# Kernel tuning notes

Measured on AMD Instinct MI355X. Metric: run time of the kernel, lower is better.

The kernel has to match this reference:

```python
import jax, jax.numpy as jnp
import numpy as np

N = 50000      # nodes
E = 800000     # edges (avg degree 16)
IN = 128       # in_channels
C = 64         # hidden_channels (per-head out channels)
H = 8          # heads


def _lin(key, fan_in, fan_out):
    kw, kb = jax.random.split(key)
    scale = 1.0 / np.sqrt(fan_in)
    W = jax.random.uniform(kw, (fan_in, fan_out), jnp.float32, -scale, scale)
    b = jax.random.uniform(kb, (fan_out,), jnp.float32, -scale, scale)
    return W, b


def setup_inputs() -> dict:
    key = jax.random.key(0)
    ks = jax.random.split(key, 16)
    inp = {
        'x': jax.random.normal(ks[0], (N, IN), jnp.float32),
        'edge_index': jax.random.randint(ks[1], (2, E), 0, N, jnp.int64),
    }
    # layer 0: IN -> H*C (concat), layer 1: H*C -> H*C (concat), layer 2: H*C -> C (heads=1)
    dims = [(IN, H * C, H * C), (H * C, H * C, H * C), (H * C, C, C)]
    k = 2
    for i, (fi, fqkv, fskip) in enumerate(dims):
        for nm, fo in (('Wq', fqkv), ('Wk', fqkv), ('Wv', fqkv), ('Ws', fskip)):
            W, b = _lin(ks[k], fi, fo)
            inp[f'{nm}{i}'] = W
            inp[f'b{nm[1]}{i}'] = b
            k += 1
    return inp


def _conv(x, src, dst, Wq, bq, Wk, bk, Wv, bv, Ws, bs, heads, ch, concat):
    n = x.shape[0]
    q = (x @ Wq + bq).reshape(n, heads, ch)   # [N,H,C]
    k = (x @ Wk + bk).reshape(n, heads, ch)
    v = (x @ Wv + bv).reshape(n, heads, ch)
    # per-edge attention logits: [E,H]
    alpha = jnp.einsum('ehc,ehc->eh', q[dst], k[src]) / (ch ** 0.5)
    # segment softmax over incoming edges of each target node
    m = jax.ops.segment_max(alpha, dst, num_segments=n)
    m = jnp.where(jnp.isfinite(m), m, 0.0)
    ea = jnp.exp(alpha - m[dst])
    denom = jax.ops.segment_sum(ea, dst, num_segments=n) + 1e-16
    attn = ea / denom[dst]                    # [E,H]
    out = jax.ops.segment_sum(attn[:, :, None] * v[src], dst, num_segments=n)  # [N,H,C]
    out = out.reshape(n, heads * ch) if concat else out.mean(axis=1)
    # root/skip connection (beta=False)
    return out + x @ Ws + bs


def reference(x, edge_index,
              Wq0, bq0, Wk0, bk0, Wv0, bv0, Ws0, bs0,
              Wq1, bq1, Wk1, bk1, Wv1, bv1, Ws1, bs1,
              Wq2, bq2, Wk2, bk2, Wv2, bv2, Ws2, bs2):
    src, dst = edge_index[0], edge_index[1]
    h = _conv(x, src, dst, Wq0, bq0, Wk0, bk0, Wv0, bv0, Ws0, bs0, H, C, True)
    h = jax.nn.relu(h)
    h = _conv(h, src, dst, Wq1, bq1, Wk1, bk1, Wv1, bv1, Ws1, bs1, H, C, True)
    h = jax.nn.relu(h)
    out = _conv(h, src, dst, Wq2, bq2, Wk2, bk2, Wv2, bv2, Ws2, bs2, 1, C, False)
    return out
```

## Files before the change

kernel.cpp:

```cpp
#include <hip/hip_runtime.h>
#include <hip/hip_fp16.h>
#include <math.h>
#include <stdio.h>


using f16x8 = __attribute__((ext_vector_type(8))) _Float16;
using f32x4 = __attribute__((ext_vector_type(4))) float;

__device__ __forceinline__ void load_lds16(const void* g, void* l) {
  __builtin_amdgcn_global_load_lds((const __attribute__((address_space(1))) void*)g,
                                   (__attribute__((address_space(3))) void*)l,
                                   16, 0, 0);
}

__device__ __forceinline__ void fp8x4_to_f32(unsigned int w, float* o4) {
#if __has_builtin(__builtin_amdgcn_cvt_pk_f32_fp8)
  auto lo = __builtin_amdgcn_cvt_pk_f32_fp8(w, false);
  auto hi = __builtin_amdgcn_cvt_pk_f32_fp8(w, true);
  o4[0] = lo[0]; o4[1] = lo[1]; o4[2] = hi[0]; o4[3] = hi[1];
#else
#pragma unroll
  for (int t = 0; t < 4; ++t) {
    unsigned int b = (w >> (8 * t)) & 0xFFu;
    unsigned short h = (unsigned short)(((b & 0x80u) << 8) | ((b & 0x7Fu) << 7));
    __half hv = *(__half*)&h;
    o4[t] = (float)hv * 256.0f;
  }
#endif
}

__device__ __forceinline__ unsigned int fp8_pack2_sw(float a, float b) {
  unsigned int r = 0;
#pragma unroll
  for (int t = 0; t < 2; ++t) {
    float f = t ? b : a;
    __half h = __float2half(f * (1.0f / 256.0f));
    unsigned short hb = *(unsigned short*)&h;
    unsigned int sign = (hb >> 8) & 0x80u;
    unsigned int mag = (hb & 0x7FFFu) + 0x40u;
    unsigned int e = (mag >> 7) & 0x7Fu;
    if ((mag >> 7) > 0x7Eu) e = 0x7Eu;
    r |= (sign | e) << (8 * t);
  }
  return r;
}

__device__ __forceinline__ uint2 fp8_pack8(const float* f) {
#if __has_builtin(__builtin_amdgcn_cvt_pk_fp8_f32)
  int w0 = __builtin_amdgcn_cvt_pk_fp8_f32(f[0], f[1], 0, false);
  w0 = __builtin_amdgcn_cvt_pk_fp8_f32(f[2], f[3], w0, true);
  int w1 = __builtin_amdgcn_cvt_pk_fp8_f32(f[4], f[5], 0, false);
  w1 = __builtin_amdgcn_cvt_pk_fp8_f32(f[6], f[7], w1, true);
  uint2 r; r.x = (unsigned)w0; r.y = (unsigned)w1; return r;
#else
  uint2 r;
  r.x = fp8_pack2_sw(f[0], f[1]) | (fp8_pack2_sw(f[2], f[3]) << 16);
  r.y = fp8_pack2_sw(f[4], f[5]) | (fp8_pack2_sw(f[6], f[7]) << 16);
  return r;
#endif
}

__global__ void prep_x_kernel(const float* __restrict__ x, __half* __restrict__ xh,
                              int* __restrict__ deg, __half* __restrict__ H,
                              int N, int Npad) {
  int t = blockIdx.x * 256 + threadIdx.x;
  if (t < N) deg[t] = 0;
  int nz = (Npad - N) * 64;
  if (t < nz) {
    f16x8 z = {};
    *(f16x8*)(H + (size_t)N * 512 + (size_t)t * 8) = z;
  }
  if (t < Npad * 16) {
    int row = t >> 4;
    f16x8 hv = {};
    if (row < N) {
      const float* g = x + (size_t)t * 8;
      float4 f0 = *(const float4*)g;
      float4 f1 = *(const float4*)(g + 4);
      hv[0] = (_Float16)f0.x; hv[1] = (_Float16)f0.y;
      hv[2] = (_Float16)f0.z; hv[3] = (_Float16)f0.w;
      hv[4] = (_Float16)f1.x; hv[5] = (_Float16)f1.y;
      hv[6] = (_Float16)f1.z; hv[7] = (_Float16)f1.w;
    }
    *(f16x8*)(xh + (size_t)t * 8) = hv;
  }
}

__global__ void degree_kernel(const int* __restrict__ dst, int* __restrict__ deg, int E) {
  int e = blockIdx.x * blockDim.x + threadIdx.x;
  if (e < E) atomicAdd(&deg[dst[e]], 1);
}

__global__ __launch_bounds__(256)
void scan_a_kernel(const int* __restrict__ deg, int* __restrict__ rowptr,
                   int* __restrict__ bsum, int n) {
  __shared__ int tmp[256];
  int t = threadIdx.x;
  int i = blockIdx.x * 256 + t;
  int v = (i < n) ? deg[i] : 0;
  tmp[t] = v;
  __syncthreads();
#pragma unroll
  for (int off = 1; off < 256; off <<= 1) {
    int u = (t >= off) ? tmp[t - off] : 0;
    __syncthreads();
    tmp[t] += u;
    __syncthreads();
  }
  if (i < n) rowptr[i + 1] = tmp[t];
  if (t == 255) bsum[blockIdx.x] = tmp[255];
}

__global__ __launch_bounds__(256)
void scan_b_kernel(int* __restrict__ bsum, int nb) {
  __shared__ int tmp[256];
  int t = threadIdx.x;
  int v = (t < nb) ? bsum[t] : 0;
  tmp[t] = v;
  __syncthreads();
#pragma unroll
  for (int off = 1; off < 256; off <<= 1) {
    int u = (t >= off) ? tmp[t - off] : 0;
    __syncthreads();
    tmp[t] += u;
    __syncthreads();
  }
  if (t < nb) bsum[t] = tmp[t] - v;
}

__global__ __launch_bounds__(256)
void scan_c_kernel(int* __restrict__ rowptr, int* __restrict__ cursor,
                   const int* __restrict__ bsum, int n) {
  int i = blockIdx.x * 256 + threadIdx.x;
  if (i < n) {
    int r = rowptr[i + 1] + bsum[blockIdx.x];
    rowptr[i + 1] = r;
    cursor[i + 1] = r;
  }
  if (i == 0) { rowptr[0] = 0; cursor[0] = 0; }
}

__global__ void scatter_kernel(const int* __restrict__ src, const int* __restrict__ dst,
                               int* __restrict__ cursor, int* __restrict__ col, int E) {
  int e = blockIdx.x * blockDim.x + threadIdx.x;
  if (e < E) {
    int pos = atomicAdd(&cursor[dst[e]], 1);
    col[pos] = src[e];
  }
}

__global__ __launch_bounds__(256)
void transpose_all_kernel(
    const float* __restrict__ Wq0, const float* __restrict__ Wk0,
    const float* __restrict__ Wv0, const float* __restrict__ Ws0,
    const float* __restrict__ Wq1, const float* __restrict__ Wk1,
    const float* __restrict__ Wv1, const float* __restrict__ Ws1,
    const float* __restrict__ Wq2, const float* __restrict__ Wk2,
    const float* __restrict__ Wv2, const float* __restrict__ Ws2,
    __half* __restrict__ Wt) {
  int z = blockIdx.z;
  int layer = z >> 2, m = z & 3;
  int K = (layer == 0) ? 128 : 512;
  int D = (layer == 2) ? 64 : 512;
  int c0 = blockIdx.x * 32, k0 = blockIdx.y * 32;
  if (c0 >= D || k0 >= K) return;
  const float* W;
  switch (z) {
    case 0: W = Wq0; break; case 1: W = Wk0; break;
    case 2: W = Wv0; break; case 3: W = Ws0; break;
    case 4: W = Wq1; break; case 5: W = Wk1; break;
    case 6: W = Wv1; break; case 7: W = Ws1; break;
    case 8: W = Wq2; break; case 9: W = Wk2; break;
    case 10: W = Wv2; break; default: W = Ws2; break;
  }
  __half* dstBase = Wt + ((layer == 0) ? 0 : (layer == 1) ? 262144 : 1310720);
  __shared__ float t[32][33];
  int tx = threadIdx.x & 31, ty = threadIdx.x >> 5;
#pragma unroll
  for (int r = 0; r < 4; ++r)
    t[ty + 8 * r][tx] = W[(size_t)(k0 + ty + 8 * r) * D + c0 + tx];
  __syncthreads();
#pragma unroll
  for (int r = 0; r < 4; ++r)
    dstBase[(size_t)(m * D + c0 + ty + 8 * r) * K + k0 + tx] =
        __float2half(t[tx][ty + 8 * r]);
}

__global__ void bias_all_kernel(
    const float* __restrict__ b0, const float* __restrict__ b1,
    const float* __restrict__ b2, const float* __restrict__ b3,
    const float* __restrict__ b4, const float* __restrict__ b5,
    const float* __restrict__ b6, const float* __restrict__ b7,
    const float* __restrict__ b8, const float* __restrict__ b9,
    const float* __restrict__ b10, const float* __restrict__ b11,
    float* __restrict__ bias_arena) {
  int z = blockIdx.x;
  int layer = z >> 2, m = z & 3;
  int D = (layer == 2) ? 64 : 512;
  const float* b;
  switch (z) {
    case 0: b = b0; break; case 1: b = b1; break;
    case 2: b = b2; break; case 3: b = b3; break;
    case 4: b = b4; break; case 5: b = b5; break;
    case 6: b = b6; break; case 7: b = b7; break;
    case 8: b = b8; break; case 9: b = b9; break;
    case 10: b = b10; break; default: b = b11; break;
  }
  float* dst = bias_arena + ((layer == 0) ? 0 : (layer == 1) ? 2048 : 4096) + m * D;
  for (int c = threadIdx.x; c < D; c += 256) dst[c] = b[c];
}

template <int LAYER>
__global__ __launch_bounds__(256, 3)
void gemm_mfma_kernel(const __half* __restrict__ Aptr,
                      const __half* __restrict__ Wt,
                      const float* __restrict__ bias,
                      __half* __restrict__ QS, __half* __restrict__ KV,
                      unsigned char* __restrict__ Q8,
                      __half* __restrict__ S16) {
  constexpr int K = (LAYER == 0) ? 128 : 512;
  constexpr int lda = (LAYER == 0) ? 128 : 512;
  constexpr int NT = (LAYER == 2) ? 2 : 16;
  constexpr int NSTEP = K / 32;
  __shared__ __align__(16) char smem_raw[49152];
  __half* sm = (__half*)smem_raw;
  int tid = threadIdx.x;
  int wave = tid >> 6, lane = tid & 63;
  int wr = wave >> 1, wc = wave & 1;
  int bid = blockIdx.x;
  int xcd = bid & 7;
  int r = bid >> 3;
  int n0 = (r % NT) * 128;
  int m0 = ((r / NT) * 8 + xcd) * 128;
  int srow = lane >> 2;
  int sslot = lane & 3;
  int skc = (sslot ^ ((srow >> 1) & 3)) << 3;
  int quad = lane >> 4, rr = lane & 15;
  int rslot = (quad ^ ((rr >> 1) & 3)) << 3;

  f32x4 acc[4][4] = {};

  auto stage = [&](int buf, int kt) {
    __half* As = sm + buf * 8192;
    __half* Bs = As + 4096;
#pragma unroll
    for (int p = 0; p < 2; ++p) {
      int rbase = wave * 32 + p * 16;
      const __half* ga = Aptr + (size_t)(m0 + rbase + srow) * lda + kt + skc;
      load_lds16(ga, &As[rbase * 32]);
    }
#pragma unroll
    for (int p = 0; p < 2; ++p) {
      int rbase = wave * 32 + p * 16;
      const __half* gb = Wt + (size_t)(n0 + rbase + srow) * K + kt + skc;
      load_lds16(gb, &Bs[rbase * 32]);
    }
  };

  stage(0, 0);
  stage(1, 32);
  stage(2, 64);

  for (int t = 0; t < NSTEP; ++t) {
    if (t + 2 < NSTEP)      asm volatile("s_waitcnt vmcnt(8)" ::: "memory");
    else if (t + 1 < NSTEP) asm volatile("s_waitcnt vmcnt(4)" ::: "memory");
    else                    asm volatile("s_waitcnt vmcnt(0)" ::: "memory");
    __builtin_amdgcn_s_barrier();

    const __half* As = sm + (t % 3) * 8192;
    const __half* Bs = As + 4096;
    f16x8 a[4], b[4];
#pragma unroll
    for (int i = 0; i < 4; ++i) {
      int row = wr * 64 + i * 16 + rr;
      a[i] = *(const f16x8*)&As[row * 32 + rslot];
    }
#pragma unroll
    for (int j = 0; j < 4; ++j) {
      int row = wc * 64 + j * 16 + rr;
      b[j] = *(const f16x8*)&Bs[row * 32 + rslot];
    }
    __builtin_amdgcn_s_setprio(1);
#pragma unroll
    for (int i = 0; i < 4; ++i)
#pragma unroll
      for (int j = 0; j < 4; ++j)
        acc[i][j] = __builtin_amdgcn_mfma_f32_16x16x32_f16(a[i], b[j], acc[i][j], 0, 0, 0);
    __builtin_amdgcn_s_setprio(0);
    __builtin_amdgcn_s_barrier();
    if (t + 3 < NSTEP) stage(t % 3, (t + 3) * 32);
  }
  __syncthreads();

  int cl = lane & 15, rb = (lane >> 4) * 4;

  if constexpr (LAYER == 2) {
    __half* S = (__half*)smem_raw;
#pragma unroll
    for (int round = 0; round < 2; ++round) {
      if (wr == round) {
#pragma unroll
        for (int i = 0; i < 4; ++i)
#pragma unroll
          for (int j = 0; j < 4; ++j) {
            int colL = wc * 64 + j * 16 + cl;
            float bj = bias[n0 + colL];
#pragma unroll
            for (int rg = 0; rg < 4; ++rg) {
              int rowL = i * 16 + rb + rg;
              S[rowL * 136 + colL] = __float2half(acc[i][j][rg] + bj);
            }
          }
      }
      __syncthreads();
#pragma unroll
      for (int it = 0; it < 4; ++it) {
        int id = it * 256 + tid;
        int rowL = id >> 4, ch = id & 15;
        int grow = m0 + round * 64 + rowL;
        int gcol = n0 + ch * 8;
        int seg = gcol >> 6, c = gcol & 63;
        __half* base = (seg == 0) ? QS + (size_t)grow * 128 + c
                     : (seg == 3) ? QS + (size_t)grow * 128 + 64 + c
                     : (seg == 1) ? KV + (size_t)grow * 128 + c
                                  : KV + (size_t)grow * 128 + 64 + c;
        *(f16x8*)base = *(const f16x8*)&S[rowL * 136 + ch * 8];
      }
      __syncthreads();
    }
  } else {
    const int msegB = n0 >> 9;
    const int cb = n0 & 511;
    if (msegB == 3) {
      __half* S = (__half*)smem_raw;
#pragma unroll
      for (int round = 0; round < 2; ++round) {
        if (wr == round) {
#pragma unroll
          for (int i = 0; i < 4; ++i)
#pragma unroll
            for (int j = 0; j < 4; ++j) {
              int colL = wc * 64 + j * 16 + cl;
              float bj = bias[n0 + colL];
#pragma unroll
              for (int rg = 0; rg < 4; ++rg) {
                int rowL = i * 16 + rb + rg;
                S[rowL * 136 + colL] = __float2half(acc[i][j][rg] + bj);
              }
            }
        }
        __syncthreads();
#pragma unroll
        for (int it = 0; it < 4; ++it) {
          int id = it * 256 + tid;
          int rowL = id >> 4, ch = id & 15;
          int grow = m0 + round * 64 + rowL;
          int colb = ch * 8;
          *(f16x8*)(S16 + (size_t)grow * 512 + cb + colb) =
              *(const f16x8*)&S[rowL * 136 + colb];
        }
        __syncthreads();
      }
    } else if (msegB == 0) {
      float* S = (float*)smem_raw;
#pragma unroll
      for (int round = 0; round < 4; ++round) {
        if (wr == (round >> 1)) {
#pragma unroll
          for (int ii = 0; ii < 2; ++ii) {
#pragma unroll
            for (int j = 0; j < 4; ++j) {
              int colL = wc * 64 + j * 16 + cl;
              float bj = bias[n0 + colL];
#pragma unroll
              for (int rg = 0; rg < 4; ++rg) {
                int rowL = ii * 16 + rb + rg;
                S[rowL * 132 + colL] = acc[(round & 1) * 2 + ii][j][rg] + bj;
              }
            }
          }
        }
        __syncthreads();
#pragma unroll
        for (int it = 0; it < 2; ++it) {
          int id = it * 256 + tid;
          int rowL = id >> 4, ch = id & 15;
          int grow = m0 + round * 32 + rowL;
          int colb = ch * 8;
          float f[8];
          f32x4 lo = *(const f32x4*)&S[rowL * 132 + colb];
          f32x4 hi = *(const f32x4*)&S[rowL * 132 + colb + 4];
          f[0] = lo[0]; f[1] = lo[1]; f[2] = lo[2]; f[3] = lo[3];
          f[4] = hi[0]; f[5] = hi[1]; f[6] = hi[2]; f[7] = hi[3];
          uint2 pk = fp8_pack8(f);
          *(uint2*)(Q8 + (size_t)grow * 512 + cb + colb) = pk;
        }
        __syncthreads();
      }
    } else {
      float* S = (float*)smem_raw;
      unsigned char* KV8 = (unsigned char*)KV;
      const int koff = (msegB == 2) ? 8 : 0;
#pragma unroll
      for (int round = 0; round < 4; ++round) {
        if (wr == (round >> 1)) {
#pragma unroll
          for (int ii = 0; ii < 2; ++ii) {
#pragma unroll
            for (int j = 0; j < 4; ++j) {
              int colL = wc * 64 + j * 16 + cl;
              float bj = bias[n0 + colL];
#pragma unroll
              for (int rg = 0; rg < 4; ++rg) {
                int rowL = ii * 16 + rb + rg;
                S[rowL * 132 + colL] = acc[(round & 1) * 2 + ii][j][rg] + bj;
              }
            }
          }
        }
        __syncthreads();
#pragma unroll
        for (int it = 0; it < 2; ++it) {
          int id = it * 256 + tid;
          int rowL = id >> 4, ch = id & 15;
          int grow = m0 + round * 32 + rowL;
          int colb = ch * 8;
          float f[8];
          f32x4 lo = *(const f32x4*)&S[rowL * 132 + colb];
          f32x4 hi = *(const f32x4*)&S[rowL * 132 + colb + 4];
          f[0] = lo[0]; f[1] = lo[1]; f[2] = lo[2]; f[3] = lo[3];
          f[4] = hi[0]; f[5] = hi[1]; f[6] = hi[2]; f[7] = hi[3];
          uint2 pk = fp8_pack8(f);
          *(uint2*)(KV8 + (size_t)grow * 1024 + ((cb + colb) >> 3) * 16 + koff) = pk;
        }
        __syncthreads();
      }
    }
  }
}

__global__ __launch_bounds__(256)
void attn_h8_kernel(const unsigned char* __restrict__ Q8,
                    const __half* __restrict__ S16,
                    const unsigned char* __restrict__ KV8,
                    const int* __restrict__ rowptr, const int* __restrict__ col,
                    __half* __restrict__ Hout, int N) {
  int n = blockIdx.x * 4 + (threadIdx.x >> 6);
  if (n >= N) return;
  int lane = threadIdx.x & 63;

  uint2 qw = *(const uint2*)(Q8 + (size_t)n * 512 + lane * 8);
  float qf[8];
  fp8x4_to_f32(qw.x, qf);
  fp8x4_to_f32(qw.y, qf + 4);

  int e0 = rowptr[n], e1 = rowptr[n + 1];
  float m = -INFINITY, l = 0.f;
  float o[8] = {};

  const uint4* KVL = (const uint4*)KV8;
  uint4 ea = {}, eb = {};
  int i = e0;
  if (i < e1)     ea = KVL[(size_t)col[i] * 64 + lane];
  if (i + 1 < e1) eb = KVL[(size_t)col[i + 1] * 64 + lane];

  while (i < e1) {
    int rem = e1 - i;
    uint4 ec = {}, ed = {};
    if (rem > 2) ec = KVL[(size_t)col[i + 2] * 64 + lane];
    if (rem > 3) ed = KVL[(size_t)col[i + 3] * 64 + lane];
    float ka[8], kb[8];
    fp8x4_to_f32(ea.x, ka); fp8x4_to_f32(ea.y, ka + 4);
    fp8x4_to_f32(eb.x, kb); fp8x4_to_f32(eb.y, kb + 4);
    float pa = 0.f, pb = 0.f;
#pragma unroll
    for (int j = 0; j < 8; ++j) { pa += ka[j] * qf[j]; pb += kb[j] * qf[j]; }
    pa += __shfl_xor(pa, 1, 64); pb += __shfl_xor(pb, 1, 64);
    pa += __shfl_xor(pa, 2, 64); pb += __shfl_xor(pb, 2, 64);
    pa += __shfl_xor(pa, 4, 64); pb += __shfl_xor(pb, 4, 64);
    float a0 = pa * 0.125f;
    float va[8];
    fp8x4_to_f32(ea.z, va); fp8x4_to_f32(ea.w, va + 4);
    if (rem > 1) {
      float vb[8];
      fp8x4_to_f32(eb.z, vb); fp8x4_to_f32(eb.w, vb + 4);
      float a1 = pb * 0.125f;
      float mn = fmaxf(m, fmaxf(a0, a1));
      float sc = __expf(m - mn);
      float ex0 = __expf(a0 - mn), ex1 = __expf(a1 - mn);
      l = l * sc + ex0 + ex1;
#pragma unroll
      for (int c = 0; c < 8; ++c)
        o[c] = o[c] * sc + ex0 * va[c] + ex1 * vb[c];
      m = mn;
    } else {
      float mn = fmaxf(m, a0);
      float sc = __expf(m - mn);
      float ex0 = __expf(a0 - mn);
      l = l * sc + ex0;
#pragma unroll
      for (int c = 0; c < 8; ++c) o[c] = o[c] * sc + ex0 * va[c];
      m = mn;
    }
    ea = ec; eb = ed;
    i += 2;
  }

  float inv = 1.f / (l + 1e-16f);
  f16x8 sv = __builtin_nontemporal_load((const f16x8*)(S16 + (size_t)n * 512 + lane * 8));
  f16x8 hv;
#pragma unroll
  for (int c = 0; c < 8; ++c) {
    float r = o[c] * inv + (float)sv[c];
    hv[c] = (_Float16)fmaxf(r, 0.f);
  }
  __builtin_nontemporal_store(hv, (f16x8*)(Hout + (size_t)n * 512 + lane * 8));
}

__global__ __launch_bounds__(256)
void attn_h1_kernel(const __half* __restrict__ QS, const __half* __restrict__ KV,
                    const int* __restrict__ rowptr, const int* __restrict__ col,
                    float* __restrict__ out, int N) {
  int n = (blockIdx.x * 256 + threadIdx.x) >> 3;
  if (n >= N) return;
  int gl = threadIdx.x & 7;
  size_t rbase = (size_t)n * 128 + gl * 8;

  f16x8 qv = __builtin_nontemporal_load((const f16x8*)(QS + rbase));
  float qf[8];
#pragma unroll
  for (int j = 0; j < 8; ++j) qf[j] = (float)qv[j];

  int e0 = rowptr[n], e1 = rowptr[n + 1];
  float m = -INFINITY, l = 0.f;
  float o[8] = {};

  f16x8 ka = {}, va = {}, kb = {}, vb = {};
  int i = e0;
  if (i < e1) {
    const __half* p = KV + (size_t)col[i] * 128 + gl * 8;
    ka = *(const f16x8*)p; va = *(const f16x8*)(p + 64);
  }
  if (i + 1 < e1) {
    const __half* p = KV + (size_t)col[i + 1] * 128 + gl * 8;
    kb = *(const f16x8*)p; vb = *(const f16x8*)(p + 64);
  }

  while (i < e1) {
    int rem = e1 - i;
    f16x8 kc = {}, vc = {}, kd = {}, vd = {};
    if (rem > 2) {
      const __half* p = KV + (size_t)col[i + 2] * 128 + gl * 8;
      kc = *(const f16x8*)p; vc = *(const f16x8*)(p + 64);
    }
    if (rem > 3) {
      const __half* p = KV + (size_t)col[i + 3] * 128 + gl * 8;
      kd = *(const f16x8*)p; vd = *(const f16x8*)(p + 64);
    }
    float pa = 0.f, pb = 0.f;
#pragma unroll
    for (int j = 0; j < 8; ++j) { pa += (float)ka[j] * qf[j]; pb += (float)kb[j] * qf[j]; }
    pa += __shfl_xor(pa, 1, 64); pb += __shfl_xor(pb, 1, 64);
    pa += __shfl_xor(pa, 2, 64); pb += __shfl_xor(pb, 2, 64);
    pa += __shfl_xor(pa, 4, 64); pb += __shfl_xor(pb, 4, 64);
    float a0 = pa * 0.125f;
    if (rem > 1) {
      float a1 = pb * 0.125f;
      float mn = fmaxf(m, fmaxf(a0, a1));
      float sc = __expf(m - mn);
      float ea = __expf(a0 - mn), eb = __expf(a1 - mn);
      l = l * sc + ea + eb;
#pragma unroll
      for (int c = 0; c < 8; ++c)
        o[c] = o[c] * sc + ea * (float)va[c] + eb * (float)vb[c];
      m = mn;
    } else {
      float mn = fmaxf(m, a0);
      float sc = __expf(m - mn);
      float ea = __expf(a0 - mn);
      l = l * sc + ea;
#pragma unroll
      for (int c = 0; c < 8; ++c) o[c] = o[c] * sc + ea * (float)va[c];
      m = mn;
    }
    ka = kc; va = vc; kb = kd; vb = vd;
    i += 2;
  }

  float inv = 1.f / (l + 1e-16f);
  f16x8 sv = __builtin_nontemporal_load((const f16x8*)(QS + rbase + 64));
  f32x4 r0, r1;
#pragma unroll
  for (int c = 0; c < 4; ++c) r0[c] = o[c] * inv + (float)sv[c];
#pragma unroll
  for (int c = 0; c < 4; ++c) r1[c] = o[c + 4] * inv + (float)sv[c + 4];
  float* op = out + (size_t)n * 64 + gl * 8;
  *(f32x4*)op = r0;
  *(f32x4*)(op + 4) = r1;
}

extern "C" void kernel_launch(void* const* d_in, const int* in_sizes, int n_in,
                              void* d_out, int out_size, void* d_ws, size_t ws_size,
                              hipStream_t stream) {
  const float* x = (const float*)d_in[0];
  const int* ei = (const int*)d_in[1];
  const int N = in_sizes[0] / 128;
  const int E = in_sizes[1] / 2;
  const int Npad = ((N + 1023) / 1024) * 1024;
  const int mtiles = Npad / 128;
  const int* srcp = ei;
  const int* dstp = ei + E;

  const float* Wq0 = (const float*)d_in[2];  const float* bq0 = (const float*)d_in[3];
  const float* Wk0 = (const float*)d_in[4];  const float* bk0 = (const float*)d_in[5];
  const float* Wv0 = (const float*)d_in[6];  const float* bv0 = (const float*)d_in[7];
  const float* Ws0 = (const float*)d_in[8];  const float* bs0 = (const float*)d_in[9];
  const float* Wq1 = (const float*)d_in[10]; const float* bq1 = (const float*)d_in[11];
  const float* Wk1 = (const float*)d_in[12]; const float* bk1 = (const float*)d_in[13];
  const float* Wv1 = (const float*)d_in[14]; const float* bv1 = (const float*)d_in[15];
  const float* Ws1 = (const float*)d_in[16]; const float* bs1 = (const float*)d_in[17];
  const float* Wq2 = (const float*)d_in[18]; const float* bq2 = (const float*)d_in[19];
  const float* Wk2 = (const float*)d_in[20]; const float* bk2 = (const float*)d_in[21];
  const float* Wv2 = (const float*)d_in[22]; const float* bv2 = (const float*)d_in[23];
  const float* Ws2 = (const float*)d_in[24]; const float* bs2 = (const float*)d_in[25];

  char* p = (char*)d_ws;
  __half* S16 = (__half*)p;              p += (size_t)Npad * 512 * 2;
  unsigned char* Q8 = (unsigned char*)p; p += (size_t)Npad * 512;
  __half* KV = (__half*)p;               p += (size_t)Npad * 1024;
  __half* H  = (__half*)p;               p += (size_t)Npad * 512 * 2;
  __half* xh = (__half*)p;               p += (size_t)Npad * 128 * 2;
  __half* Wt = (__half*)p;               p += (size_t)1441792 * 2;
  float* bias_arena = (float*)p;         p += 4352 * 4;
  int* deg    = (int*)p;                 p += (size_t)N * 4;
  int* rowptr = (int*)p;                 p += (size_t)(N + 1) * 4;
  int* cursor = (int*)p;                 p += (size_t)(N + 1) * 4;
  int* colv   = (int*)p;                 p += (size_t)E * 4;
  int* bsum   = (int*)p;                 p += 256 * 4;
  size_t need = p - (char*)d_ws;
  if (ws_size < need) {
    fprintf(stderr, "kernel_launch: ws_size=%zu < need=%zu — aborting cleanly\n",
            ws_size, need);
    return;
  }

  const int nscan = (N + 255) / 256;

  transpose_all_kernel<<<dim3(16, 16, 12), 256, 0, stream>>>(
      Wq0, Wk0, Wv0, Ws0, Wq1, Wk1, Wv1, Ws1, Wq2, Wk2, Wv2, Ws2, Wt);
  bias_all_kernel<<<12, 256, 0, stream>>>(
      bq0, bk0, bv0, bs0, bq1, bk1, bv1, bs1, bq2, bk2, bv2, bs2, bias_arena);
  prep_x_kernel<<<(Npad * 16 + 255) / 256, 256, 0, stream>>>(x, xh, deg, H, N, Npad);

  degree_kernel<<<(E + 255) / 256, 256, 0, stream>>>(dstp, deg, E);
  scan_a_kernel<<<nscan, 256, 0, stream>>>(deg, rowptr, bsum, N);
  scan_b_kernel<<<1, 256, 0, stream>>>(bsum, nscan);
  scan_c_kernel<<<nscan, 256, 0, stream>>>(rowptr, cursor, bsum, N);
  scatter_kernel<<<(E + 255) / 256, 256, 0, stream>>>(srcp, dstp, cursor, colv, E);

  __half* Wt0 = Wt;
  __half* Wt1 = Wt + 262144;
  __half* Wt2 = Wt + 1310720;

  gemm_mfma_kernel<0><<<mtiles * 16, 256, 0, stream>>>(
      xh, Wt0, bias_arena, S16, KV, Q8, S16);
  attn_h8_kernel<<<(N + 3) / 4, 256, 0, stream>>>(Q8, S16, (const unsigned char*)KV,
                                                  rowptr, colv, H, N);

  gemm_mfma_kernel<1><<<mtiles * 16, 256, 0, stream>>>(
      H, Wt1, bias_arena + 2048, S16, KV, Q8, S16);
  attn_h8_kernel<<<(N + 3) / 4, 256, 0, stream>>>(Q8, S16, (const unsigned char*)KV,
                                                  rowptr, colv, H, N);

  gemm_mfma_kernel<2><<<mtiles * 2, 256, 0, stream>>>(
      H, Wt2, bias_arena + 4096, S16, KV, Q8, S16);
  attn_h1_kernel<<<(N + 31) / 32, 256, 0, stream>>>(S16, KV, rowptr, colv,
                                                    (float*)d_out, N);
}
```

Measured before the change: 702.3 us.

## Load GEMM operands directly into registers instead of LDS triple-buffering

Removes the global-to-LDS triple-buffered staging, its waitcnt/barrier synchronization and the swizzled LDS reads. Each wave now loads its MFMA A/B fragments straight from global memory into registers, with register double-buffering and a fully unrolled k-loop. LDS shrinks to what the epilogue needs, and launch bounds drop to 2 blocks per CU to leave room for the extra registers. Without LDS the waves sharing a tile no longer share operand loads, so redundant global/L2 traffic rises and latency hiding relies on one step of register prefetch.

```diff
diff --git a/kernel.cpp b/kernel.cpp
--- a/kernel.cpp
+++ b/kernel.cpp
@@ -6,12 +6,6 @@
 
 using f16x8 = __attribute__((ext_vector_type(8))) _Float16;
 using f32x4 = __attribute__((ext_vector_type(4))) float;
-
-__device__ __forceinline__ void load_lds16(const void* g, void* l) {
-  __builtin_amdgcn_global_load_lds((const __attribute__((address_space(1))) void*)g,
-                                   (__attribute__((address_space(3))) void*)l,
-                                   16, 0, 0);
-}
 
 __device__ __forceinline__ void fp8x4_to_f32(unsigned int w, float* o4) {
 #if __has_builtin(__builtin_amdgcn_cvt_pk_f32_fp8)
@@ -211,7 +205,7 @@
 }
 
 template <int LAYER>
-__global__ __launch_bounds__(256, 3)
+__global__ __launch_bounds__(256, 2)
 void gemm_mfma_kernel(const __half* __restrict__ Aptr,
                       const __half* __restrict__ Wt,
                       const float* __restrict__ bias,
@@ -222,8 +216,7 @@
   constexpr int lda = (LAYER == 0) ? 128 : 512;
   constexpr int NT = (LAYER == 2) ? 2 : 16;
   constexpr int NSTEP = K / 32;
-  __shared__ __align__(16) char smem_raw[49152];
-  __half* sm = (__half*)smem_raw;
+  __shared__ __align__(16) char smem_raw[18432];
   int tid = threadIdx.x;
   int wave = tid >> 6, lane = tid & 63;
   int wr = wave >> 1, wc = wave & 1;
@@ -232,63 +225,37 @@
   int r = bid >> 3;
   int n0 = (r % NT) * 128;
   int m0 = ((r / NT) * 8 + xcd) * 128;
-  int srow = lane >> 2;
-  int sslot = lane & 3;
-  int skc = (sslot ^ ((srow >> 1) & 3)) << 3;
   int quad = lane >> 4, rr = lane & 15;
-  int rslot = (quad ^ ((rr >> 1) & 3)) << 3;
+
+  const __half* Abase = Aptr + (size_t)(m0 + wr * 64 + rr) * lda + quad * 8;
+  const __half* Bbase = Wt + (size_t)(n0 + wc * 64 + rr) * K + quad * 8;
 
   f32x4 acc[4][4] = {};
-
-  auto stage = [&](int buf, int kt) {
-    __half* As = sm + buf * 8192;
-    __half* Bs = As + 4096;
-#pragma unroll
-    for (int p = 0; p < 2; ++p) {
-      int rbase = wave * 32 + p * 16;
-      const __half* ga = Aptr + (size_t)(m0 + rbase + srow) * lda + kt + skc;
-      load_lds16(ga, &As[rbase * 32]);
-    }
-#pragma unroll
-    for (int p = 0; p < 2; ++p) {
-      int rbase = wave * 32 + p * 16;
-      const __half* gb = Wt + (size_t)(n0 + rbase + srow) * K + kt + skc;
-      load_lds16(gb, &Bs[rbase * 32]);
-    }
-  };
-
-  stage(0, 0);
-  stage(1, 32);
-  stage(2, 64);
-
+  f16x8 a[4], b[4], an[4], bn[4];
+
+#pragma unroll
+  for (int i = 0; i < 4; ++i) {
+    a[i] = *(const f16x8*)(Abase + (size_t)(i * 16) * lda);
+    b[i] = *(const f16x8*)(Bbase + (size_t)(i * 16) * K);
+  }
+
+#pragma unroll
   for (int t = 0; t < NSTEP; ++t) {
-    if (t + 2 < NSTEP)      asm volatile("s_waitcnt vmcnt(8)" ::: "memory");
-    else if (t + 1 < NSTEP) asm volatile("s_waitcnt vmcnt(4)" ::: "memory");
-    else                    asm volatile("s_waitcnt vmcnt(0)" ::: "memory");
-    __builtin_amdgcn_s_barrier();
-
-    const __half* As = sm + (t % 3) * 8192;
-    const __half* Bs = As + 4096;
-    f16x8 a[4], b[4];
-#pragma unroll
-    for (int i = 0; i < 4; ++i) {
-      int row = wr * 64 + i * 16 + rr;
-      a[i] = *(const f16x8*)&As[row * 32 + rslot];
-    }
-#pragma unroll
-    for (int j = 0; j < 4; ++j) {
-      int row = wc * 64 + j * 16 + rr;
-      b[j] = *(const f16x8*)&Bs[row * 32 + rslot];
-    }
-    __builtin_amdgcn_s_setprio(1);
+    if (t + 1 < NSTEP) {
+      int kn = (t + 1) * 32;
+#pragma unroll
+      for (int i = 0; i < 4; ++i) {
+        an[i] = *(const f16x8*)(Abase + (size_t)(i * 16) * lda + kn);
+        bn[i] = *(const f16x8*)(Bbase + (size_t)(i * 16) * K + kn);
+      }
+    }
 #pragma unroll
     for (int i = 0; i < 4; ++i)
 #pragma unroll
       for (int j = 0; j < 4; ++j)
         acc[i][j] = __builtin_amdgcn_mfma_f32_16x16x32_f16(a[i], b[j], acc[i][j], 0, 0, 0);
-    __builtin_amdgcn_s_setprio(0);
-    __builtin_amdgcn_s_barrier();
-    if (t + 3 < NSTEP) stage(t % 3, (t + 3) * 32);
+#pragma unroll
+    for (int i = 0; i < 4; ++i) { a[i] = an[i]; b[i] = bn[i]; }
   }
   __syncthreads();
 
```

Measured after the change: 1.063 ms. +51.3%, slower.
